# Optimization experiments

Hardware: AMD Instinct MI355X
Metric: run time of the kernel (lower is better)

## Reference

```python
import jax, jax.numpy as jnp
import numpy as np

B, T, C = 4, 2048, 1024
H, D = 16, 64
SCALE = D ** -0.5


def setup_inputs() -> dict:
    key = jax.random.key(0)
    ks = jax.random.split(key, 5)
    s = 0.02
    return {
        "hidden_states": jax.random.normal(ks[0], (B, T, C), dtype=jnp.float32),
        "attention_mask": jnp.ones((B, T), dtype=jnp.int32),
        "Wq": jax.random.normal(ks[1], (C, H * D), dtype=jnp.float32) * s,
        "Wk": jax.random.normal(ks[2], (C, H * D), dtype=jnp.float32) * s,
        "Wv": jax.random.normal(ks[3], (C, H * D), dtype=jnp.float32) * s,
        "Wo": jax.random.normal(ks[4], (H * D, C), dtype=jnp.float32) * s,
        "bo": jnp.zeros((C,), dtype=jnp.float32),
    }


def reference(hidden_states, attention_mask, Wq, Wk, Wv, Wo, bo):
    b, t, _ = hidden_states.shape
    # projections -> (B, H, T, D)
    q = (hidden_states @ Wq).reshape(b, t, H, D).transpose(0, 2, 1, 3)
    k = (hidden_states @ Wk).reshape(b, t, H, D).transpose(0, 2, 1, 3)
    v = (hidden_states @ Wv).reshape(b, t, H, D).transpose(0, 2, 1, 3)
    # scores (B, H, Tq, Tk)
    scores = jnp.einsum("bhqd,bhkd->bhqk", q, k) * SCALE
    mask = attention_mask[:, None, None, :]  # (B,1,1,T), dim==2 branch
    scores = jnp.where(mask == 0, -jnp.inf, scores)
    probs = jax.nn.softmax(scores, axis=-1)
    out = jnp.einsum("bhqk,bhkd->bhqd", probs, v)
    out = out.transpose(0, 2, 1, 3).reshape(b, t, H * D)
    return out @ Wo + bo
```

## Files before the change

### kernel.cpp

```cpp
#include <hip/hip_runtime.h>
#include <hip/hip_bf16.h>

#define B_ 4
#define T_ 2048
#define C_ 1024
#define H_ 16
#define D_ 64
#define SCALE_ 0.125f
#define L2E 1.4426950408889634f
#define SE (SCALE_ * L2E)

typedef __attribute__((ext_vector_type(8))) short bf16x8;
typedef __attribute__((ext_vector_type(4))) float f32x4;

__device__ __forceinline__ unsigned short f2bf(float f) {
    union { float f; unsigned u; } v; v.f = f;
    unsigned r = v.u + 0x7fff + ((v.u >> 16) & 1);
    return (unsigned short)(r >> 16);
}

__device__ __forceinline__ unsigned pk2bf(float a, float b) {
    __hip_bfloat162 t = __float22bfloat162_rn(make_float2(a, b));
    union { __hip_bfloat162 h; unsigned u; } c; c.h = t;
    return c.u;
}

__device__ __forceinline__ void gl_lds16(const unsigned short* g, unsigned short* l) {
    __builtin_amdgcn_global_load_lds(
        (const __attribute__((address_space(1))) void*)g,
        (__attribute__((address_space(3))) void*)l,
        16, 0, 0);
}

__global__ void cvt_hs_kernel(const float4* __restrict__ in, ushort4* __restrict__ out) {
    int i = blockIdx.x * 256 + threadIdx.x;
    float4 v = in[i];
    ushort4 o;
    o.x = f2bf(v.x); o.y = f2bf(v.y); o.z = f2bf(v.z); o.w = f2bf(v.w);
    out[i] = o;
}

__global__ void wtrans_kernel(const float* __restrict__ Wq, const float* __restrict__ Wk,
                              const float* __restrict__ Wv, const float* __restrict__ Wo,
                              unsigned short* __restrict__ Wqkv_t, unsigned short* __restrict__ Wo_t) {
    __shared__ float tile[64][65];
    int mtx = blockIdx.y;
    const float* W = (mtx == 0) ? Wq : (mtx == 1) ? Wk : (mtx == 2) ? Wv : Wo;
    unsigned short* Out = (mtx < 3) ? (Wqkv_t + (size_t)mtx * 1024 * 1024) : Wo_t;
    int tl = blockIdx.x;
    int tx = tl & 15, ty = tl >> 4;
    int t = threadIdx.x;
    int col = t & 63, rb = t >> 6;
#pragma unroll
    for (int rr = 0; rr < 16; ++rr) {
        int r = rb * 16 + rr;
        tile[r][col] = W[(size_t)(ty * 64 + r) * 1024 + tx * 64 + col];
    }
    __syncthreads();
#pragma unroll
    for (int rr = 0; rr < 16; ++rr) {
        int r = rb * 16 + rr;
        Out[(size_t)(tx * 64 + r) * 1024 + ty * 64 + col] = f2bf(tile[col][r]);
    }
}

__global__ __launch_bounds__(256) void gemm_qkv_kernel(
    const unsigned short* __restrict__ A, const unsigned short* __restrict__ Bt,
    unsigned short* __restrict__ Qg, unsigned short* __restrict__ Kf, unsigned short* __restrict__ Vf) {
    __shared__ __align__(16) unsigned short As[128 * 32];
    __shared__ __align__(16) unsigned short Bs[128 * 32];
    const int tid = threadIdx.x;
    const int w = tid >> 6, lane = tid & 63;
    const int quad = lane >> 4, l16 = lane & 15;
    const int m0 = blockIdx.y * 128, n0 = blockIdx.x * 128;
    const int mw = (w >> 1) * 64, nw = (w & 1) * 64;
    const int K = 1024;
    const int srow = lane >> 2;
    const int scol = (lane & 3) * 8;

    const f32x4 fzero = {0.f, 0.f, 0.f, 0.f};
    f32x4 acc[4][4];
#pragma unroll
    for (int i = 0; i < 4; ++i)
#pragma unroll
        for (int j = 0; j < 4; ++j) acc[i][j] = fzero;

    for (int k0 = 0; k0 < K; k0 += 32) {
        gl_lds16(A + (size_t)(m0 + w * 32 + srow) * K + k0 + scol,       As + (w * 32) * 32);
        gl_lds16(A + (size_t)(m0 + w * 32 + 16 + srow) * K + k0 + scol,  As + (w * 32 + 16) * 32);
        gl_lds16(Bt + (size_t)(n0 + w * 32 + srow) * K + k0 + scol,      Bs + (w * 32) * 32);
        gl_lds16(Bt + (size_t)(n0 + w * 32 + 16 + srow) * K + k0 + scol, Bs + (w * 32 + 16) * 32);
        __syncthreads();
        bf16x8 a[4], b[4];
#pragma unroll
        for (int i = 0; i < 4; ++i)
            a[i] = *(const bf16x8*)(As + (mw + i * 16 + l16) * 32 + quad * 8);
#pragma unroll
        for (int j = 0; j < 4; ++j)
            b[j] = *(const bf16x8*)(Bs + (nw + j * 16 + l16) * 32 + quad * 8);
#pragma unroll
        for (int i = 0; i < 4; ++i)
#pragma unroll
            for (int j = 0; j < 4; ++j)
                acc[i][j] = __builtin_amdgcn_mfma_f32_16x16x32_bf16(a[i], b[j], acc[i][j], 0, 0, 0);
        __syncthreads();
    }

#pragma unroll
    for (int j = 0; j < 4; ++j) {
        int gn = n0 + nw + j * 16 + l16;
        int tensor = gn >> 10;
        int nl = gn & 1023;
        int hh = nl >> 6, dd = nl & 63;
#pragma unroll
        for (int i = 0; i < 4; ++i) {
            int gmb = m0 + mw + i * 16 + quad * 4;
            int bb = gmb >> 11;
            size_t bhh = (size_t)(bb * 16 + hh);
            if (tensor == 0) {
#pragma unroll
                for (int r = 0; r < 4; ++r) {
                    int tt = (gmb + r) & 2047;
                    Qg[(bhh * 2048 + tt) * 64 + dd] = f2bf(acc[i][j][r]);
                }
            } else if (tensor == 1) {
#pragma unroll
                for (int r = 0; r < 4; ++r) {
                    int tt = (gmb + r) & 2047;
                    Kf[bhh * 131072 + (size_t)(tt >> 4) * 1024 + (dd >> 5) * 512 +
                       (((dd >> 3) & 3) * 16 + (tt & 15)) * 8 + (dd & 7)] = f2bf(acc[i][j][r]);
                }
            } else {
                int tt = gmb & 2047;
                ushort4 v4;
                v4.x = f2bf(acc[i][j][0]); v4.y = f2bf(acc[i][j][1]);
                v4.z = f2bf(acc[i][j][2]); v4.w = f2bf(acc[i][j][3]);
                *(ushort4*)(Vf + bhh * 131072 + (size_t)(tt >> 5) * 2048 + (dd >> 4) * 512 +
                            (((tt >> 3) & 3) * 16 + (dd & 15)) * 8 + (tt & 7)) = v4;
            }
        }
    }
}

__global__ __launch_bounds__(256) void attn_kernel(
    const unsigned short* __restrict__ Qg, const unsigned short* __restrict__ Kf,
    const unsigned short* __restrict__ Vf, const int* __restrict__ mask,
    unsigned short* __restrict__ AO) {
    __shared__ __align__(16) unsigned short Pbuf[4][2048];
    __shared__ float li_lds[4][32];

    const int tid = threadIdx.x;
    const int w = tid >> 6, lane = tid & 63;
    const int quad = lane >> 4, l16 = lane & 15;
    const int bid = blockIdx.x;
    const int bh = (bid & 7) * 8 + ((bid >> 7) & 7);
    const int qt = (bid >> 3) & 15;
    const int b = bh >> 4, h = bh & 15;
    const size_t bh_td = (size_t)bh * (2048 * 64);
    const int q0w = qt * 128 + w * 32;

    bf16x8 aq[2][2];
#pragma unroll
    for (int qi = 0; qi < 2; ++qi)
#pragma unroll
        for (int hh = 0; hh < 2; ++hh)
            aq[qi][hh] = *(const bf16x8*)(Qg + bh_td + (size_t)(q0w + qi * 16 + l16) * 64 + hh * 32 + quad * 8);

    const unsigned short* Kp = Kf + bh_td + lane * 8;
    const unsigned short* Vp = Vf + bh_td + lane * 8;
    const int* mrow = mask + b * 2048;

    const f32x4 fzero = {0.f, 0.f, 0.f, 0.f};
    f32x4 po[2][4];
#pragma unroll
    for (int qi = 0; qi < 2; ++qi)
#pragma unroll
        for (int nd = 0; nd < 4; ++nd) po[qi][nd] = fzero;
    float li[2] = {0.f, 0.f};

    for (int k0 = 0; k0 < 2048; k0 += 64) {
        const int tb = (k0 >> 4) * 1024;
        bf16x8 ka0[4], ka1[4];
#pragma unroll
        for (int kt = 0; kt < 4; ++kt) {
            ka0[kt] = *(const bf16x8*)(Kp + tb + kt * 1024);
            ka1[kt] = *(const bf16x8*)(Kp + tb + kt * 1024 + 512);
        }
        bf16x8 bv[2][4];
#pragma unroll
        for (int c = 0; c < 2; ++c)
#pragma unroll
            for (int nd = 0; nd < 4; ++nd)
                bv[c][nd] = *(const bf16x8*)(Vp + ((k0 >> 5) + c) * 2048 + nd * 512);

#pragma unroll
        for (int kt = 0; kt < 4; ++kt) {
            int4 mv = *(const int4*)(mrow + k0 + kt * 16 + quad * 4);
            float mb0 = mv.x ? 0.f : -1e30f;
            float mb1 = mv.y ? 0.f : -1e30f;
            float mb2 = mv.z ? 0.f : -1e30f;
            float mb3 = mv.w ? 0.f : -1e30f;
            int pidx = ((((kt & 1) << 1) | (quad >> 1)) * 16 + l16) * 8 + (quad & 1) * 4;
#pragma unroll
            for (int qi = 0; qi < 2; ++qi) {
                f32x4 st = __builtin_amdgcn_mfma_f32_16x16x32_bf16(ka0[kt], aq[qi][0], fzero, 0, 0, 0);
                st = __builtin_amdgcn_mfma_f32_16x16x32_bf16(ka1[kt], aq[qi][1], st, 0, 0, 0);
                float p0 = __builtin_amdgcn_exp2f(st[0] * SE + mb0);
                float p1 = __builtin_amdgcn_exp2f(st[1] * SE + mb1);
                float p2 = __builtin_amdgcn_exp2f(st[2] * SE + mb2);
                float p3 = __builtin_amdgcn_exp2f(st[3] * SE + mb3);
                li[qi] += (p0 + p1) + (p2 + p3);
                uint2 pk; pk.x = pk2bf(p0, p1); pk.y = pk2bf(p2, p3);
                *(uint2*)(Pbuf[w] + (qi * 2 + (kt >> 1)) * 512 + pidx) = pk;
            }
        }

        asm volatile("s_waitcnt lgkmcnt(0)" ::: "memory");

#pragma unroll
        for (int c = 0; c < 2; ++c)
#pragma unroll
            for (int qi = 0; qi < 2; ++qi) {
                bf16x8 ap = *(const bf16x8*)(Pbuf[w] + (qi * 2 + c) * 512 + lane * 8);
#pragma unroll
                for (int nd = 0; nd < 4; ++nd)
                    po[qi][nd] = __builtin_amdgcn_mfma_f32_16x16x32_bf16(ap, bv[c][nd], po[qi][nd], 0, 0, 0);
            }
    }

#pragma unroll
    for (int qi = 0; qi < 2; ++qi) {
        li[qi] += __shfl_xor(li[qi], 16, 64);
        li[qi] += __shfl_xor(li[qi], 32, 64);
        if (quad == 0) li_lds[w][qi * 16 + l16] = li[qi];
    }
    asm volatile("s_waitcnt lgkmcnt(0)" ::: "memory");
    float linv[2][4];
#pragma unroll
    for (int qi = 0; qi < 2; ++qi)
#pragma unroll
        for (int r = 0; r < 4; ++r)
            linv[qi][r] = __builtin_amdgcn_rcpf(li_lds[w][qi * 16 + quad * 4 + r]);

#pragma unroll
    for (int qi = 0; qi < 2; ++qi)
#pragma unroll
        for (int r = 0; r < 4; ++r) {
            int q = q0w + qi * 16 + quad * 4 + r;
            size_t ob = (size_t)(b * 2048 + q) * 1024 + h * 64;
#pragma unroll
            for (int nd = 0; nd < 4; ++nd)
                AO[ob + nd * 16 + l16] = f2bf(po[qi][nd][r] * linv[qi][r]);
        }
}

__global__ __launch_bounds__(256) void gemm_out_kernel(
    const unsigned short* __restrict__ A, const unsigned short* __restrict__ Bt,
    const float* __restrict__ bo, float* __restrict__ out) {
    __shared__ __align__(16) unsigned short As[128 * 32];
    __shared__ __align__(16) unsigned short Bs[128 * 32];
    const int tid = threadIdx.x;
    const int w = tid >> 6, lane = tid & 63;
    const int quad = lane >> 4, l16 = lane & 15;
    const int m0 = blockIdx.y * 128, n0 = blockIdx.x * 128;
    const int mw = (w >> 1) * 64, nw = (w & 1) * 64;
    const int K = 1024;
    const int srow = lane >> 2;
    const int scol = (lane & 3) * 8;

    const f32x4 fzero = {0.f, 0.f, 0.f, 0.f};
    f32x4 acc[4][4];
#pragma unroll
    for (int i = 0; i < 4; ++i)
#pragma unroll
        for (int j = 0; j < 4; ++j) acc[i][j] = fzero;

    for (int k0 = 0; k0 < K; k0 += 32) {
        gl_lds16(A + (size_t)(m0 + w * 32 + srow) * K + k0 + scol,       As + (w * 32) * 32);
        gl_lds16(A + (size_t)(m0 + w * 32 + 16 + srow) * K + k0 + scol,  As + (w * 32 + 16) * 32);
        gl_lds16(Bt + (size_t)(n0 + w * 32 + srow) * K + k0 + scol,      Bs + (w * 32) * 32);
        gl_lds16(Bt + (size_t)(n0 + w * 32 + 16 + srow) * K + k0 + scol, Bs + (w * 32 + 16) * 32);
        __syncthreads();
        bf16x8 a[4], b[4];
#pragma unroll
        for (int i = 0; i < 4; ++i)
            a[i] = *(const bf16x8*)(As + (mw + i * 16 + l16) * 32 + quad * 8);
#pragma unroll
        for (int j = 0; j < 4; ++j)
            b[j] = *(const bf16x8*)(Bs + (nw + j * 16 + l16) * 32 + quad * 8);
#pragma unroll
        for (int i = 0; i < 4; ++i)
#pragma unroll
            for (int j = 0; j < 4; ++j)
                acc[i][j] = __builtin_amdgcn_mfma_f32_16x16x32_bf16(a[i], b[j], acc[i][j], 0, 0, 0);
        __syncthreads();
    }

#pragma unroll
    for (int j = 0; j < 4; ++j) {
        int gn = n0 + nw + j * 16 + l16;
        float bias = bo[gn];
#pragma unroll
        for (int i = 0; i < 4; ++i) {
            int gmb = m0 + mw + i * 16 + quad * 4;
#pragma unroll
            for (int r = 0; r < 4; ++r)
                out[(size_t)(gmb + r) * 1024 + gn] = acc[i][j][r] + bias;
        }
    }
}

extern "C" void kernel_launch(void* const* d_in, const int* in_sizes, int n_in,
                              void* d_out, int out_size, void* d_ws, size_t ws_size,
                              hipStream_t stream) {
    const float* hs  = (const float*)d_in[0];
    const int* mask  = (const int*)d_in[1];
    const float* Wq  = (const float*)d_in[2];
    const float* Wk  = (const float*)d_in[3];
    const float* Wv  = (const float*)d_in[4];
    const float* Wo  = (const float*)d_in[5];
    const float* bo  = (const float*)d_in[6];
    float* out = (float*)d_out;

    char* ws = (char*)d_ws;
    unsigned short* hs_bf = (unsigned short*)(ws);
    unsigned short* wqkv  = (unsigned short*)(ws + 16777216);
    unsigned short* wo_t  = (unsigned short*)(ws + 23068672);
    unsigned short* Qg    = (unsigned short*)(ws + 25165824);
    unsigned short* Kf    = (unsigned short*)(ws + 41943040);
    unsigned short* Vf    = (unsigned short*)(ws + 58720256);
    unsigned short* AO    = (unsigned short*)(ws + 75497472);

    cvt_hs_kernel<<<8192, 256, 0, stream>>>((const float4*)hs, (ushort4*)hs_bf);
    wtrans_kernel<<<dim3(256, 4), 256, 0, stream>>>(Wq, Wk, Wv, Wo, wqkv, wo_t);
    gemm_qkv_kernel<<<dim3(24, 64), 256, 0, stream>>>(hs_bf, wqkv, Qg, Kf, Vf);
    attn_kernel<<<1024, 256, 0, stream>>>(Qg, Kf, Vf, mask, AO);
    gemm_out_kernel<<<dim3(8, 64), 256, 0, stream>>>(AO, wo_t, bo, out);
}
```

Before: 304.8 us.

## Fold softmax scale into Q, skip mask math for full tiles, sum rows via MFMA

Pre-multiplies Q by scale*log2e in the projection epilogue, so the attention loop no longer multiplies each score. Adds a wave ballot that takes a branch without mask loads or adds when all 64 keys are unmasked. Computes the softmax row sums with an extra MFMA against a ones vector instead of VALU adds, shuffles and an LDS round trip. In exchange it adds MFMA work and rounds the row sums from bf16 P values, and Q is now rounded to bf16 after scaling.

```diff
diff --git a/kernel.cpp b/kernel.cpp
--- a/kernel.cpp
+++ b/kernel.cpp
@@ -121,7 +121,7 @@
 #pragma unroll
                 for (int r = 0; r < 4; ++r) {
                     int tt = (gmb + r) & 2047;
-                    Qg[(bhh * 2048 + tt) * 64 + dd] = f2bf(acc[i][j][r]);
+                    Qg[(bhh * 2048 + tt) * 64 + dd] = f2bf(acc[i][j][r] * SE);
                 }
             } else if (tensor == 1) {
 #pragma unroll
@@ -147,7 +147,6 @@
     const unsigned short* __restrict__ Vf, const int* __restrict__ mask,
     unsigned short* __restrict__ AO) {
     __shared__ __align__(16) unsigned short Pbuf[4][2048];
-    __shared__ float li_lds[4][32];
 
     const int tid = threadIdx.x;
     const int w = tid >> 6, lane = tid & 63;
@@ -170,13 +169,19 @@
     const unsigned short* Vp = Vf + bh_td + lane * 8;
     const int* mrow = mask + b * 2048;
 
+    bf16x8 vones;
+#pragma unroll
+    for (int i = 0; i < 8; ++i) vones[i] = (short)0x3F80;
+
     const f32x4 fzero = {0.f, 0.f, 0.f, 0.f};
     f32x4 po[2][4];
-#pragma unroll
-    for (int qi = 0; qi < 2; ++qi)
+    f32x4 pl[2];
+#pragma unroll
+    for (int qi = 0; qi < 2; ++qi) {
+        pl[qi] = fzero;
 #pragma unroll
         for (int nd = 0; nd < 4; ++nd) po[qi][nd] = fzero;
-    float li[2] = {0.f, 0.f};
+    }
 
     for (int k0 = 0; k0 < 2048; k0 += 64) {
         const int tb = (k0 >> 4) * 1024;
@@ -186,6 +191,49 @@
             ka0[kt] = *(const bf16x8*)(Kp + tb + kt * 1024);
             ka1[kt] = *(const bf16x8*)(Kp + tb + kt * 1024 + 512);
         }
+
+        int mk = mrow[k0 + lane];
+        bool allok = (__ballot(mk != 0) == 0xFFFFFFFFFFFFFFFFull);
+
+        if (allok) {
+#pragma unroll
+            for (int kt = 0; kt < 4; ++kt) {
+                int pidx = ((((kt & 1) << 1) | (quad >> 1)) * 16 + l16) * 8 + (quad & 1) * 4;
+#pragma unroll
+                for (int qi = 0; qi < 2; ++qi) {
+                    f32x4 st = __builtin_amdgcn_mfma_f32_16x16x32_bf16(ka0[kt], aq[qi][0], fzero, 0, 0, 0);
+                    st = __builtin_amdgcn_mfma_f32_16x16x32_bf16(ka1[kt], aq[qi][1], st, 0, 0, 0);
+                    float p0 = __builtin_amdgcn_exp2f(st[0]);
+                    float p1 = __builtin_amdgcn_exp2f(st[1]);
+                    float p2 = __builtin_amdgcn_exp2f(st[2]);
+                    float p3 = __builtin_amdgcn_exp2f(st[3]);
+                    uint2 pk; pk.x = pk2bf(p0, p1); pk.y = pk2bf(p2, p3);
+                    *(uint2*)(Pbuf[w] + (qi * 2 + (kt >> 1)) * 512 + pidx) = pk;
+                }
+            }
+        } else {
+#pragma unroll
+            for (int kt = 0; kt < 4; ++kt) {
+                int4 mv = *(const int4*)(mrow + k0 + kt * 16 + quad * 4);
+                float mb0 = mv.x ? 0.f : -1e30f;
+                float mb1 = mv.y ? 0.f : -1e30f;
+                float mb2 = mv.z ? 0.f : -1e30f;
+                float mb3 = mv.w ? 0.f : -1e30f;
+                int pidx = ((((kt & 1) << 1) | (quad >> 1)) * 16 + l16) * 8 + (quad & 1) * 4;
+#pragma unroll
+                for (int qi = 0; qi < 2; ++qi) {
+                    f32x4 st = __builtin_amdgcn_mfma_f32_16x16x32_bf16(ka0[kt], aq[qi][0], fzero, 0, 0, 0);
+                    st = __builtin_amdgcn_mfma_f32_16x16x32_bf16(ka1[kt], aq[qi][1], st, 0, 0, 0);
+                    float p0 = __builtin_amdgcn_exp2f(st[0] + mb0);
+                    float p1 = __builtin_amdgcn_exp2f(st[1] + mb1);
+                    float p2 = __builtin_amdgcn_exp2f(st[2] + mb2);
+                    float p3 = __builtin_amdgcn_exp2f(st[3] + mb3);
+                    uint2 pk; pk.x = pk2bf(p0, p1); pk.y = pk2bf(p2, p3);
+                    *(uint2*)(Pbuf[w] + (qi * 2 + (kt >> 1)) * 512 + pidx) = pk;
+                }
+            }
+        }
+
         bf16x8 bv[2][4];
 #pragma unroll
         for (int c = 0; c < 2; ++c)
@@ -193,28 +241,6 @@
             for (int nd = 0; nd < 4; ++nd)
                 bv[c][nd] = *(const bf16x8*)(Vp + ((k0 >> 5) + c) * 2048 + nd * 512);
 
-#pragma unroll
-        for (int kt = 0; kt < 4; ++kt) {
-            int4 mv = *(const int4*)(mrow + k0 + kt * 16 + quad * 4);
-            float mb0 = mv.x ? 0.f : -1e30f;
-            float mb1 = mv.y ? 0.f : -1e30f;
-            float mb2 = mv.z ? 0.f : -1e30f;
-            float mb3 = mv.w ? 0.f : -1e30f;
-            int pidx = ((((kt & 1) << 1) | (quad >> 1)) * 16 + l16) * 8 + (quad & 1) * 4;
-#pragma unroll
-            for (int qi = 0; qi < 2; ++qi) {
-                f32x4 st = __builtin_amdgcn_mfma_f32_16x16x32_bf16(ka0[kt], aq[qi][0], fzero, 0, 0, 0);
-                st = __builtin_amdgcn_mfma_f32_16x16x32_bf16(ka1[kt], aq[qi][1], st, 0, 0, 0);
-                float p0 = __builtin_amdgcn_exp2f(st[0] * SE + mb0);
-                float p1 = __builtin_amdgcn_exp2f(st[1] * SE + mb1);
-                float p2 = __builtin_amdgcn_exp2f(st[2] * SE + mb2);
-                float p3 = __builtin_amdgcn_exp2f(st[3] * SE + mb3);
-                li[qi] += (p0 + p1) + (p2 + p3);
-                uint2 pk; pk.x = pk2bf(p0, p1); pk.y = pk2bf(p2, p3);
-                *(uint2*)(Pbuf[w] + (qi * 2 + (kt >> 1)) * 512 + pidx) = pk;
-            }
-        }
-
         asm volatile("s_waitcnt lgkmcnt(0)" ::: "memory");
 
 #pragma unroll
@@ -225,32 +251,20 @@
 #pragma unroll
                 for (int nd = 0; nd < 4; ++nd)
                     po[qi][nd] = __builtin_amdgcn_mfma_f32_16x16x32_bf16(ap, bv[c][nd], po[qi][nd], 0, 0, 0);
+                pl[qi] = __builtin_amdgcn_mfma_f32_16x16x32_bf16(ap, vones, pl[qi], 0, 0, 0);
             }
     }
 
 #pragma unroll
-    for (int qi = 0; qi < 2; ++qi) {
-        li[qi] += __shfl_xor(li[qi], 16, 64);
-        li[qi] += __shfl_xor(li[qi], 32, 64);
-        if (quad == 0) li_lds[w][qi * 16 + l16] = li[qi];
-    }
-    asm volatile("s_waitcnt lgkmcnt(0)" ::: "memory");
-    float linv[2][4];
-#pragma unroll
     for (int qi = 0; qi < 2; ++qi)
 #pragma unroll
-        for (int r = 0; r < 4; ++r)
-            linv[qi][r] = __builtin_amdgcn_rcpf(li_lds[w][qi * 16 + quad * 4 + r]);
-
-#pragma unroll
-    for (int qi = 0; qi < 2; ++qi)
-#pragma unroll
         for (int r = 0; r < 4; ++r) {
+            float linv = __builtin_amdgcn_rcpf(pl[qi][r]);
             int q = q0w + qi * 16 + quad * 4 + r;
             size_t ob = (size_t)(b * 2048 + q) * 1024 + h * 64;
 #pragma unroll
             for (int nd = 0; nd < 4; ++nd)
-                AO[ob + nd * 16 + l16] = f2bf(po[qi][nd][r] * linv[qi][r]);
+                AO[ob + nd * 16 + l16] = f2bf(po[qi][nd][r] * linv);
         }
 }
 
```

After: 296.5 us. -2.7%, faster.
